# Optimization experiments

Measured on AMD Instinct MI355X. Metric: run time of the kernel, lower is better.

Reference implementation:

```python
import jax, jax.numpy as jnp
import numpy as np

# Module config (matches init_kwargs)
K_W, K_H = 3, 3
C_IN, C_OUT = 64, 64
B, W_IN, H_IN = 8, 32, 32
J = K_W * K_H * C_IN  # flattened patch length, torch layout (c_in, k_w, k_h)


def setup_inputs() -> dict:
    key = jax.random.key(0)
    k_x, k_w = jax.random.split(key)
    x = jax.random.normal(k_x, (B, W_IN, H_IN, C_IN), dtype=jnp.float32)
    # reset_parameters: randint{0,1} * 2 - 1 -> weights in {-1, +1}
    weights = jax.random.randint(k_w, (C_OUT, J), 0, 2).astype(jnp.float32) * 2.0 - 1.0
    return {"input": x, "weights": weights}


def reference(input, weights):
    b, w_in, h_in, c_in = input.shape
    pw, ph = K_W // 2, K_H // 2
    # F.pad(..., value=-1) pads the two spatial dims, channels untouched
    xp = jnp.pad(input, ((0, 0), (pw, pw), (ph, ph), (0, 0)), constant_values=-1.0)
    # torch .unfold(1,k_w,1).unfold(2,k_h,1) -> (B, W, H, c_in, k_w, k_h)
    patches = jnp.stack(
        [jnp.stack([xp[:, u:u + w_in, v:v + h_in, :] for v in range(K_H)], axis=-1)
         for u in range(K_W)],
        axis=-2,
    )  # (B, W, H, c_in, k_w, k_h)
    # flatten patch, then view flat axis as (k_w, k_h*c_in) exactly like the
    # torch reshape([-1, k_w, k_h*c_in]) (a pure regrouping of the flat axis)
    u = patches.reshape(b * w_in * h_in, K_W, K_H * c_in)  # (N, k_w, k_h*c_in)
    wv = weights.reshape(C_OUT, K_W, K_H * c_in)            # (A, k_w, k_h*c_in)
    # einsum('bj,aj->baj') then sum over the k_w-sized chunk axis == contract u
    inter = jnp.einsum('nug,aug->nag', u, wv)               # (N, c_out, k_h*c_in)
    # majority vote: clamp to [-1,1], scale by 3, reduce
    out = jnp.sum(jnp.clip(inter, -1.0, 1.0) * 3.0, axis=-1)  # (N, c_out)
    return out.reshape(b, w_in, h_in, C_OUT)
```

## Files before the change

### kernel.cpp

```cpp
#include <hip/hip_runtime.h>


typedef unsigned int u32;
typedef float f4 __attribute__((ext_vector_type(4)));
typedef _Float16 h8 __attribute__((ext_vector_type(8)));
typedef __fp16 hp2 __attribute__((ext_vector_type(2)));
typedef u32 uu2 __attribute__((ext_vector_type(2)));
typedef int i4 __attribute__((ext_vector_type(4)));

#define HS    19
#define PLANE (64 * HS)
#define NP    16

__device__ __forceinline__ float clip1(float s) {
    return __builtin_amdgcn_fmed3f(s, -1.0f, 1.0f);
}

__global__ __launch_bounds__(192) void prep_kernel(const float* __restrict__ w,
                                                   u32* __restrict__ M32) {
    const int a = blockIdx.x, G = threadIdx.x;
    const float w1 = w[a * 576 + G];
    const float w2 = w[a * 576 + 192 + G];
    const float w3 = w[a * 576 + 384 + G];
    const int q = ((w1 * w2 < 0.f) ? 2 : 0) + ((w1 * w3 < 0.f) ? 1 : 0);
    const u32 s1 = (w1 < 0.f) ? 0xBC00u : 0x3C00u;
    const u32 v0 = (q == 0) ? s1 : 0u, v1 = (q == 1) ? s1 : 0u;
    const u32 v2 = (q == 2) ? s1 : 0u, v3 = (q == 3) ? s1 : 0u;
    M32[a * 384 + G * 2 + 0] = v0 | (v1 << 16);
    M32[a * 384 + G * 2 + 1] = v2 | (v3 << 16);
}

template <int R0>
__device__ __forceinline__ void phaseA_12(const float* __restrict__ xt,
                                          u32* __restrict__ yb,
                                          int ci0, int p) {
#pragma unroll
    for (int d = 0; d < 12; ++d) {
        const int r    = (R0 + d) % 9;
        const int cinc = (R0 + d) / 9;
        const int uv1 = r;           const int cA = 0;
        const int uv2 = (r + 3) % 9; const int cB = 21 + (r + 3) / 9;
        const int uv3 = (r + 6) % 9; const int cC = 42 + (r + 6) / 9;
        const int ci = ci0 + cinc;
        const float x1 = xt[(uv1 / 3) * PLANE + (ci + cA) * HS + p + (uv1 % 3)];
        const float x2 = xt[(uv2 / 3) * PLANE + (ci + cB) * HS + p + (uv2 % 3)];
        const float x3 = xt[(uv3 / 3) * PLANE + (ci + cC) * HS + p + (uv3 % 3)];
        const float sp = x1 + x2, sm = x1 - x2;
        const float y0 = clip1(sp + x3), y1 = clip1(sp - x3);
        const float y2 = clip1(sm + x3), y3 = clip1(sm - x3);
        hp2 lo = __builtin_amdgcn_cvt_pkrtz(y0, y1);
        hp2 hi = __builtin_amdgcn_cvt_pkrtz(y2, y3);
        uu2 pr;
        pr.x = __builtin_bit_cast(u32, lo);
        pr.y = __builtin_bit_cast(u32, hi);
        const int G = 9 * ci + r;
        *(uu2*)&yb[(G * NP + p) * 2] = pr;
    }
}

__global__ __launch_bounds__(256) void maj3_kernel(const float* __restrict__ x,
                                                   const u32* __restrict__ M32,
                                                   float* __restrict__ out) {
    __shared__ float xt[3 * PLANE];
    __shared__ u32  yb[192 * NP * 2];

    const int tid   = threadIdx.x;
    const int lane  = tid & 63;
    const int wid   = tid >> 6;
    const int blk   = blockIdx.x;
    const int hhalf = blk & 1;
    const int bw    = blk >> 1;
    const int bimg  = bw >> 5, wrow = bw & 31;
    const int h0    = hhalf * NP;

    {
        const int c = tid & 63, slot = tid >> 6;
        const float* xb = x + (bimg * 32 * 32) * 64 + c;
#pragma unroll 1
        for (int i = slot; i < 54; i += 4) {
            const int u = i / 18, hh = i % 18;
            const int wx = wrow - 1 + u, hx = h0 - 1 + hh;
            float v = -1.0f;
            if ((unsigned)wx < 32u && (unsigned)hx < 32u)
                v = xb[(wx * 32 + hx) * 64];
            xt[u * PLANE + c * HS + hh] = v;
        }
    }
    __syncthreads();

    {
        const int p = lane & 15, sub = lane >> 4;
        const int s = wid * 4 + sub;
        const int ci0 = (4 * s) / 3;
        const int sel = s % 3;
        if (sel == 0)      phaseA_12<0>(xt, yb, ci0, p);
        else if (sel == 1) phaseA_12<3>(xt, yb, ci0, p);
        else               phaseA_12<6>(xt, yb, ci0, p);
    }
    __syncthreads();

    {
        const int p16 = lane & 15, sub = lane >> 4;
        const int a0  = wid * 16;
        const u32* mp = M32 + (a0 + p16) * 384 + sub * 4;
        i4 af[24];
#pragma unroll
        for (int st = 0; st < 24; ++st)
            af[st] = *(const i4*)(mp + st * 16);

        f4 acc = {0.f, 0.f, 0.f, 0.f};
#pragma unroll
        for (int st = 0; st < 24; ++st) {
            const int Ga = st * 8 + sub * 2;
            uu2 b0 = *(const uu2*)&yb[(Ga * NP + p16) * 2];
            uu2 b1 = *(const uu2*)&yb[((Ga + 1) * NP + p16) * 2];
            i4 bi;
            bi.x = (int)b0.x; bi.y = (int)b0.y;
            bi.z = (int)b1.x; bi.w = (int)b1.y;
            acc = __builtin_amdgcn_mfma_f32_16x16x32_f16(
                      __builtin_bit_cast(h8, af[st]),
                      __builtin_bit_cast(h8, bi), acc, 0, 0, 0);
        }

        const int n = bw * 32 + h0 + p16;
        float* op = out + n * 64 + a0 + sub * 4;
        f4 o;
#pragma unroll
        for (int r = 0; r < 4; ++r) o[r] = 3.0f * acc[r];
        *(f4*)op = o;
    }
}

extern "C" void kernel_launch(void* const* d_in, const int* in_sizes, int n_in,
                              void* d_out, int out_size, void* d_ws, size_t ws_size,
                              hipStream_t stream) {
    const float* x = (const float*)d_in[0];
    const float* w = (const float*)d_in[1];
    float* out = (float*)d_out;
    u32* M32 = (u32*)d_ws;
    prep_kernel<<<64, 192, 0, stream>>>(w, M32);
    maj3_kernel<<<512, 256, 0, stream>>>(x, M32, out);
}
```

Before: 69.89 us.

## Hoist global loads ahead of LDS staging and interleave yb layout for b128 reads

Input tile loads are fully unrolled into registers and the MFMA A-fragment (weight) loads are issued before the first barrier, so global latency overlaps instead of being serialized across phases. The yb LDS buffer is re-laid out so that two consecutive G pairs are contiguous, letting the MFMA B operand be fetched with a single 128-bit LDS read instead of two 64-bit reads. launch_bounds is also raised to request two blocks per CU. This increases register pressure (14 floats plus 24 i4 fragments live across the barriers), which could limit occupancy or cause spills.

```diff
diff --git a/kernel.cpp b/kernel.cpp
--- a/kernel.cpp
+++ b/kernel.cpp
@@ -14,6 +14,10 @@
 
 __device__ __forceinline__ float clip1(float s) {
     return __builtin_amdgcn_fmed3f(s, -1.0f, 1.0f);
+}
+
+__device__ __forceinline__ int ybi(int G, int p) {
+    return ((G >> 1) * NP + p) * 4 + (G & 1) * 2;
 }
 
 __global__ __launch_bounds__(192) void prep_kernel(const float* __restrict__ w,
@@ -54,15 +58,15 @@
         pr.x = __builtin_bit_cast(u32, lo);
         pr.y = __builtin_bit_cast(u32, hi);
         const int G = 9 * ci + r;
-        *(uu2*)&yb[(G * NP + p) * 2] = pr;
+        *(uu2*)&yb[ybi(G, p)] = pr;
     }
 }
 
-__global__ __launch_bounds__(256) void maj3_kernel(const float* __restrict__ x,
-                                                   const u32* __restrict__ M32,
-                                                   float* __restrict__ out) {
+__global__ __launch_bounds__(256, 2) void maj3_kernel(
+        const float* __restrict__ x, const u32* __restrict__ M32,
+        float* __restrict__ out) {
     __shared__ float xt[3 * PLANE];
-    __shared__ u32  yb[192 * NP * 2];
+    __shared__ u32  yb[96 * NP * 4];
 
     const int tid   = threadIdx.x;
     const int lane  = tid & 63;
@@ -73,50 +77,54 @@
     const int bimg  = bw >> 5, wrow = bw & 31;
     const int h0    = hhalf * NP;
 
-    {
-        const int c = tid & 63, slot = tid >> 6;
-        const float* xb = x + (bimg * 32 * 32) * 64 + c;
-#pragma unroll 1
-        for (int i = slot; i < 54; i += 4) {
-            const int u = i / 18, hh = i % 18;
-            const int wx = wrow - 1 + u, hx = h0 - 1 + hh;
-            float v = -1.0f;
-            if ((unsigned)wx < 32u && (unsigned)hx < 32u)
-                v = xb[(wx * 32 + hx) * 64];
-            xt[u * PLANE + c * HS + hh] = v;
+    const int p16 = lane & 15, sub = lane >> 4;
+    const int a0  = wid * 16;
+
+    const int c = lane;
+    const float* xb = x + (bimg * 32 * 32) * 64 + c;
+    float vs[14];
+#pragma unroll
+    for (int j = 0; j < 14; ++j) {
+        const int i = wid + 4 * j;
+        const int u = i / 18, hh = i - u * 18;
+        const int wx = wrow - 1 + u, hx = h0 - 1 + hh;
+        float v = -1.0f;
+        if (i < 54 && (unsigned)wx < 32u && (unsigned)hx < 32u)
+            v = xb[(wx * 32 + hx) * 64];
+        vs[j] = v;
+    }
+
+    const u32* mp = M32 + (a0 + p16) * 384 + sub * 4;
+    i4 af[24];
+#pragma unroll
+    for (int st = 0; st < 24; ++st)
+        af[st] = *(const i4*)(mp + st * 16);
+
+#pragma unroll
+    for (int j = 0; j < 14; ++j) {
+        const int i = wid + 4 * j;
+        if (i < 54) {
+            const int u = i / 18, hh = i - u * 18;
+            xt[u * PLANE + c * HS + hh] = vs[j];
         }
     }
     __syncthreads();
 
     {
-        const int p = lane & 15, sub = lane >> 4;
         const int s = wid * 4 + sub;
         const int ci0 = (4 * s) / 3;
         const int sel = s % 3;
-        if (sel == 0)      phaseA_12<0>(xt, yb, ci0, p);
-        else if (sel == 1) phaseA_12<3>(xt, yb, ci0, p);
-        else               phaseA_12<6>(xt, yb, ci0, p);
+        if (sel == 0)      phaseA_12<0>(xt, yb, ci0, p16);
+        else if (sel == 1) phaseA_12<3>(xt, yb, ci0, p16);
+        else               phaseA_12<6>(xt, yb, ci0, p16);
     }
     __syncthreads();
 
     {
-        const int p16 = lane & 15, sub = lane >> 4;
-        const int a0  = wid * 16;
-        const u32* mp = M32 + (a0 + p16) * 384 + sub * 4;
-        i4 af[24];
-#pragma unroll
-        for (int st = 0; st < 24; ++st)
-            af[st] = *(const i4*)(mp + st * 16);
-
         f4 acc = {0.f, 0.f, 0.f, 0.f};
 #pragma unroll
         for (int st = 0; st < 24; ++st) {
-            const int Ga = st * 8 + sub * 2;
-            uu2 b0 = *(const uu2*)&yb[(Ga * NP + p16) * 2];
-            uu2 b1 = *(const uu2*)&yb[((Ga + 1) * NP + p16) * 2];
-            i4 bi;
-            bi.x = (int)b0.x; bi.y = (int)b0.y;
-            bi.z = (int)b1.x; bi.w = (int)b1.y;
+            i4 bi = *(const i4*)&yb[((st * 4 + sub) * NP + p16) * 4];
             acc = __builtin_amdgcn_mfma_f32_16x16x32_f16(
                       __builtin_bit_cast(h8, af[st]),
                       __builtin_bit_cast(h8, bi), acc, 0, 0, 0);
```

After: 66.17 us. 1.06x faster.
